# Performance work log

Hardware: AMD Instinct MI355X
Metric: run time of the kernel (lower is better)

Reference implementation:

```python
import jax, jax.numpy as jnp
import numpy as np

E = 256
H = 512
LN_EPS = 1e-5
NORM_EPS = 1e-12


def setup_inputs() -> dict:
    key = jax.random.key(0)
    ks = jax.random.split(key, 8)
    B, N, M = 8, 128, 128
    track_features = jax.random.normal(ks[0], (B, N, E), dtype=jnp.float32)
    det_features = jax.random.normal(ks[1], (B, M, E), dtype=jnp.float32)
    # MLP params (torch Linear default init style: uniform, but values irrelevant for correctness harness)
    lim1 = 1.0 / np.sqrt(3 * E)
    W1 = jax.random.uniform(ks[2], (3 * E, H), minval=-lim1, maxval=lim1, dtype=jnp.float32)
    b1 = jax.random.uniform(ks[3], (H,), minval=-lim1, maxval=lim1, dtype=jnp.float32)
    gamma = jnp.ones((H,), dtype=jnp.float32)
    beta = jnp.zeros((H,), dtype=jnp.float32)
    lim2 = 1.0 / np.sqrt(H)
    W2 = jax.random.uniform(ks[4], (H, 1), minval=-lim2, maxval=lim2, dtype=jnp.float32)
    b2 = jax.random.uniform(ks[5], (1,), minval=-lim2, maxval=lim2, dtype=jnp.float32)
    return {"track_features": track_features, "det_features": det_features,
            "W1": W1, "b1": b1, "gamma": gamma, "beta": beta, "W2": W2, "b2": b2}


def _l2_normalize(x):
    # F.normalize(x, dim=-1): x / max(||x||_2, eps)
    n = jnp.sqrt(jnp.sum(x * x, axis=-1, keepdims=True))
    return x / jnp.maximum(n, NORM_EPS)


def reference(track_features, det_features, W1, b1, gamma, beta, W2, b2):
    t = _l2_normalize(track_features)   # (B, N, E)
    d = _l2_normalize(det_features)     # (B, M, E)
    tb = t[:, :, None, :]               # (B, N, 1, E)
    db = d[:, None, :, :]               # (B, 1, M, E)
    B, N, _ = t.shape
    M = d.shape[1]
    diff = jnp.abs(tb - db)                                  # (B, N, M, E)
    pair = jnp.concatenate([jnp.broadcast_to(tb, (B, N, M, E)),
                            jnp.broadcast_to(db, (B, N, M, E)),
                            diff], axis=-1)                  # (B, N, M, 3E)
    h = jnp.einsum('bnme,eh->bnmh', pair, W1) + b1           # (B, N, M, H)
    mu = jnp.mean(h, axis=-1, keepdims=True)
    var = jnp.mean((h - mu) ** 2, axis=-1, keepdims=True)
    h = (h - mu) * jax.lax.rsqrt(var + LN_EPS) * gamma + beta
    h = h * jax.nn.sigmoid(h)                                # SiLU
    out = jnp.einsum('bnmh,ho->bnmo', h, W2)[..., 0] + b2[0]  # (B, N, M)
    return out
```

## Files before the change

### kernel.cpp

```cpp
#include <hip/hip_runtime.h>
#include <hip/hip_bf16.h>
#include <cstdint>

typedef __bf16 bf16x8 __attribute__((ext_vector_type(8)));
typedef __bf16 bf16x2 __attribute__((ext_vector_type(2)));
typedef float f32x4 __attribute__((ext_vector_type(4)));
typedef float f32x2 __attribute__((ext_vector_type(2)));

#define E_DIM 256
#define H_DIM 512

static __device__ __forceinline__ unsigned pkbf(float a, float b) {
    bf16x2 h;
    h[0] = (__bf16)a;
    h[1] = (__bf16)b;
    return __builtin_bit_cast(unsigned, h);
}

__global__ __launch_bounds__(512, 2)
void prep_kernel(const float* __restrict__ track, const float* __restrict__ det,
                 const float* __restrict__ W1, const float* __restrict__ b1,
                 float* __restrict__ P, float* __restrict__ Q,
                 __bf16* __restrict__ W1cc, float* __restrict__ sclT,
                 float* __restrict__ sclD, float* __restrict__ out) {
    __shared__ __align__(16) __bf16 Ash[16 * 256];
    int tid = threadIdx.x;
    int blk = blockIdx.x;

    if (blk >= 288) {
        int u = (blk - 288) * 512 + tid;
        float4 z = {0.f, 0.f, 0.f, 0.f};
#pragma unroll
        for (int i = 0; i < 4; ++i)
            ((float4*)out)[u + 8192 * i] = z;
        return;
    }
    if (blk >= 256) {
        int u = (blk - 256) * 512 + tid;
        int j = u & 3;
        int h = (u >> 2) & 511;
        int c = u >> 11;
        const float* src = W1 + (size_t)(512 + c * 32 + j * 8) * H_DIM + h;
        uint4 v;
        v.x = pkbf(src[0],                 src[(size_t)1 * H_DIM]);
        v.y = pkbf(src[(size_t)2 * H_DIM], src[(size_t)3 * H_DIM]);
        v.z = pkbf(src[(size_t)4 * H_DIM], src[(size_t)5 * H_DIM]);
        v.w = pkbf(src[(size_t)6 * H_DIM], src[(size_t)7 * H_DIM]);
        *(uint4*)(W1cc + ((size_t)(c * 512 + h) * 32 + j * 8)) = v;
        return;
    }

    int lane = tid & 63;
    int wave = tid >> 6;
    int lq   = lane >> 4;
    int lc   = lane & 15;
    int l5   = lane & 31;

    int mat  = blk >> 7;
    int rowg = (blk >> 1) & 63;
    int half = blk & 1;
    int r0   = rowg * 16;
    int h0   = half * 256;
    const float* src = mat ? det : track;

    {
        int row = wave * 2 + (lane >> 5);
        const float* gp = src + (size_t)(r0 + row) * E_DIM + l5 * 8;
        float4 x0 = *(const float4*)gp;
        float4 x1 = *(const float4*)(gp + 4);
        float ss = x0.x*x0.x + x0.y*x0.y + x0.z*x0.z + x0.w*x0.w
                 + x1.x*x1.x + x1.y*x1.y + x1.z*x1.z + x1.w*x1.w;
#pragma unroll
        for (int off = 16; off > 0; off >>= 1) ss += __shfl_xor(ss, off);
        float st = 1.0f / fmaxf(sqrtf(ss), 1e-12f);
        if (half == 0 && l5 == 0) (mat ? sclD : sclT)[r0 + row] = st;
        uint4 v;
        v.x = pkbf(x0.x * st, x0.y * st);
        v.y = pkbf(x0.z * st, x0.w * st);
        v.z = pkbf(x1.x * st, x1.y * st);
        v.w = pkbf(x1.z * st, x1.w * st);
        int cc = l5 >> 2, j = l5 & 3;
        *(uint4*)&Ash[(size_t)(cc * 64 + j * 16 + row) * 8] = v;
    }
    __syncthreads();

    int hB = h0 + wave * 32 + lc;
    const float* wb = W1 + (size_t)(mat * 256) * H_DIM + hB;
    float wf[2][8];
#pragma unroll
    for (int ht = 0; ht < 2; ++ht)
#pragma unroll
        for (int i = 0; i < 8; ++i)
            wf[ht][i] = wb[(size_t)(lq * 8 + i) * H_DIM + ht * 16];

    f32x4 acc[2];
    acc[0] = (f32x4){0.f, 0.f, 0.f, 0.f};
    acc[1] = (f32x4){0.f, 0.f, 0.f, 0.f};

#pragma unroll
    for (int c = 0; c < 8; ++c) {
        bf16x8 cw[2];
#pragma unroll
        for (int ht = 0; ht < 2; ++ht) {
            uint4 u;
            u.x = pkbf(wf[ht][0], wf[ht][1]);
            u.y = pkbf(wf[ht][2], wf[ht][3]);
            u.z = pkbf(wf[ht][4], wf[ht][5]);
            u.w = pkbf(wf[ht][6], wf[ht][7]);
            cw[ht] = __builtin_bit_cast(bf16x8, u);
        }
        if (c < 7) {
            const float* nb = wb + (size_t)((c + 1) * 32 + lq * 8) * H_DIM;
#pragma unroll
            for (int ht = 0; ht < 2; ++ht)
#pragma unroll
                for (int i = 0; i < 8; ++i)
                    wf[ht][i] = nb[(size_t)i * H_DIM + ht * 16];
        }
        bf16x8 af = *(const bf16x8*)&Ash[(size_t)(c * 64 + lane) * 8];
#pragma unroll
        for (int ht = 0; ht < 2; ++ht)
            acc[ht] = __builtin_amdgcn_mfma_f32_16x16x32_bf16(cw[ht], af, acc[ht], 0, 0, 0);
    }

    float* dst = mat ? Q : P;
#pragma unroll
    for (int ht = 0; ht < 2; ++ht) {
        int h = h0 + wave * 32 + ht * 16 + lq * 4;
        f32x4 o = acc[ht];
        if (!mat) o += *(const f32x4*)&b1[h];
        *(f32x4*)&dst[(size_t)(r0 + lc) * H_DIM + h] = o;
    }
}

__global__ __launch_bounds__(512, 4)
void main_kernel(const float* __restrict__ track, const float* __restrict__ det,
                 const __bf16* __restrict__ W1cc,
                 const float* __restrict__ P, const float* __restrict__ Q,
                 const float* __restrict__ sclT, const float* __restrict__ sclD,
                 const float* __restrict__ gamma, const float* __restrict__ beta,
                 const float* __restrict__ W2, const float* __restrict__ b2,
                 float* __restrict__ out) {
    __shared__ __align__(16) char SMEM[44032];
    __bf16* Ash  = (__bf16*)SMEM;
    float*  LNr1 = (float*)(SMEM + 32768);
    float*  LNr2 = (float*)(SMEM + 35072);
    float*  AS   = (float*)(SMEM + 37376);
    float*  BS   = (float*)(SMEM + 37632);
    float*  Gs   = (float*)(SMEM + 37888);
    float*  Bs   = (float*)(SMEM + 39936);
    float*  Ws   = (float*)(SMEM + 41984);

    int tid  = threadIdx.x;
    int lane = tid & 63;
    int wave = tid >> 6;
    int lq   = lane >> 4;
    int lc   = lane & 15;

    int i   = blockIdx.x;
    int xcd = i & 7;
    int t8  = (i >> 3) & 31;
    int b   = i >> 8;
    int n0  = ((xcd >> 1) * 4 + (t8 >> 3)) * 8;
    int m0  = ((xcd & 1) * 8 + (t8 & 7)) * 8;
    int gn  = b * 128 + n0;
    int gm  = b * 128 + m0;

    float b2v = b2[0];
    Gs[tid] = gamma[tid];
    Bs[tid] = beta[tid];
    Ws[tid] = W2[tid];

    const uint4* Wg = (const uint4*)W1cc;
    int hb = wave * 64 + lc;
    bf16x8 bwA[4], bwB[4];
#pragma unroll
    for (int ht = 0; ht < 4; ++ht)
        bwA[ht] = __builtin_bit_cast(bf16x8, Wg[(hb + ht * 16) * 4 + lq]);

    int k0 = wave * 32 + lq * 8;
    int ml = lane & 7;
    float sd = sclD[gm + ml];
    const float* dr = det + (size_t)(gm + ml) * E_DIM + k0;
    float4 d0 = *(const float4*)dr;
    float4 d1 = *(const float4*)(dr + 4);
#pragma unroll
    for (int r = 0; r < 4; ++r) {
        int nl = r * 2 + (lc >> 3);
        float st = sclT[gn + nl];
        const float* tr = track + (size_t)(gn + nl) * E_DIM + k0;
        float4 t0 = *(const float4*)tr;
        float4 t1 = *(const float4*)(tr + 4);
        uint4 v;
        v.x = pkbf(fabsf(t0.x * st - d0.x * sd), fabsf(t0.y * st - d0.y * sd));
        v.y = pkbf(fabsf(t0.z * st - d0.z * sd), fabsf(t0.w * st - d0.w * sd));
        v.z = pkbf(fabsf(t1.x * st - d1.x * sd), fabsf(t1.y * st - d1.y * sd));
        v.w = pkbf(fabsf(t1.z * st - d1.z * sd), fabsf(t1.w * st - d1.w * sd));
        *(uint4*)&Ash[(size_t)(r * 512 + wave * 64 + lane) * 8] = v;
    }

    const float* Pb = P + (size_t)gn * H_DIM;
    const float* Qb = Q + (size_t)gm * H_DIM;
    f32x4 acc[4][4];
    {
        f32x4 qv[4];
#pragma unroll
        for (int ht = 0; ht < 4; ++ht)
            qv[ht] = *(const f32x4*)&Qb[(size_t)ml * H_DIM + wave * 64 + ht * 16 + lq * 4];
#pragma unroll
        for (int pt = 0; pt < 4; ++pt) {
            int n = pt * 2 + (lc >> 3);
#pragma unroll
            for (int ht = 0; ht < 4; ++ht) {
                f32x4 pv = *(const f32x4*)&Pb[(size_t)n * H_DIM + wave * 64 + ht * 16 + lq * 4];
                acc[pt][ht] = pv + qv[ht];
            }
        }
    }
    __syncthreads();

#pragma unroll 2
    for (int c = 0; c < 8; ++c) {
        bf16x8* cur = (c & 1) ? bwB : bwA;
        bf16x8* nxt = (c & 1) ? bwA : bwB;
        int c1 = (c + 1) & 7;
#pragma unroll
        for (int ht = 0; ht < 4; ++ht)
            nxt[ht] = __builtin_bit_cast(bf16x8, Wg[c1 * 2048 + (hb + ht * 16) * 4 + lq]);
        __builtin_amdgcn_s_setprio(1);
#pragma unroll
        for (int pt = 0; pt < 4; ++pt) {
            bf16x8 af = *(const bf16x8*)&Ash[(size_t)((pt * 8 + c) * 64 + lane) * 8];
#pragma unroll
            for (int ht = 0; ht < 4; ++ht)
                acc[pt][ht] = __builtin_amdgcn_mfma_f32_16x16x32_bf16(cur[ht], af, acc[pt][ht], 0, 0, 0);
        }
        __builtin_amdgcn_s_setprio(0);
    }

#pragma unroll
    for (int pt = 0; pt < 4; ++pt) {
        f32x2 s1v = (f32x2){0.f, 0.f}, s2v = (f32x2){0.f, 0.f};
#pragma unroll
        for (int ht = 0; ht < 4; ++ht) {
#pragma unroll
            for (int hf = 0; hf < 2; ++hf) {
                f32x2 v = (f32x2){acc[pt][ht][hf * 2], acc[pt][ht][hf * 2 + 1]};
                s1v += v;
                s2v += v * v;
            }
        }
        float s1 = s1v[0] + s1v[1];
        float s2 = s2v[0] + s2v[1];
        s1 += __shfl_xor(s1, 16); s2 += __shfl_xor(s2, 16);
        s1 += __shfl_xor(s1, 32); s2 += __shfl_xor(s2, 32);
        if (lq == 0) {
            LNr1[(pt * 16 + lc) * 9 + wave] = s1;
            LNr2[(pt * 16 + lc) * 9 + wave] = s2;
        }
    }
    __syncthreads();
    {
        int p = tid >> 3, w = tid & 7;
        float s1 = LNr1[p * 9 + w];
        float s2 = LNr2[p * 9 + w];
        s1 += __shfl_xor(s1, 1); s2 += __shfl_xor(s2, 1);
        s1 += __shfl_xor(s1, 2); s2 += __shfl_xor(s2, 2);
        s1 += __shfl_xor(s1, 4); s2 += __shfl_xor(s2, 4);
        if (w == 0) {
            float mu  = s1 * (1.0f / 512.0f);
            float var = s2 * (1.0f / 512.0f) - mu * mu;
            float rs  = rsqrtf(var + 1e-5f);
            AS[p] = rs;
            BS[p] = -mu * rs;
        }
    }
    __syncthreads();

    float as[4], bs[4];
#pragma unroll
    for (int pt = 0; pt < 4; ++pt) { as[pt] = AS[pt * 16 + lc]; bs[pt] = BS[pt * 16 + lc]; }
    f32x2 cav[4];
#pragma unroll
    for (int pt = 0; pt < 4; ++pt) cav[pt] = (f32x2){0.f, 0.f};
#pragma unroll
    for (int ht = 0; ht < 4; ++ht) {
        int h = wave * 64 + ht * 16 + lq * 4;
        f32x4 g  = *(const f32x4*)&Gs[h];
        f32x4 bb = *(const f32x4*)&Bs[h];
        f32x4 w  = *(const f32x4*)&Ws[h];
#pragma unroll
        for (int pt = 0; pt < 4; ++pt) {
            f32x2 a2  = (f32x2){as[pt], as[pt]};
            f32x2 b2p = (f32x2){bs[pt], bs[pt]};
#pragma unroll
            for (int hf = 0; hf < 2; ++hf) {
                f32x2 v  = (f32x2){acc[pt][ht][hf * 2], acc[pt][ht][hf * 2 + 1]};
                f32x2 gg = (f32x2){g[hf * 2],  g[hf * 2 + 1]};
                f32x2 bv = (f32x2){bb[hf * 2], bb[hf * 2 + 1]};
                f32x2 wv = (f32x2){w[hf * 2],  w[hf * 2 + 1]};
                f32x2 x  = (v * a2 + b2p) * gg + bv;
                f32x2 xw = x * wv;
                f32x2 e, sg;
                e[0]  = __expf(-x[0]);
                e[1]  = __expf(-x[1]);
                sg[0] = __builtin_amdgcn_rcpf(1.0f + e[0]);
                sg[1] = __builtin_amdgcn_rcpf(1.0f + e[1]);
                cav[pt] += xw * sg;
            }
        }
    }
#pragma unroll
    for (int pt = 0; pt < 4; ++pt) {
        float cg = cav[pt][0] + cav[pt][1];
        cg += __shfl_xor(cg, 16);
        cg += __shfl_xor(cg, 32);
        if (lq == 0) {
            if (wave == 0) cg += b2v;
            int n = pt * 2 + (lc >> 3);
            int m = lc & 7;
            atomicAdd(&out[(size_t)(gn + n) * 128 + m0 + m], cg);
        }
    }
}

extern "C" void kernel_launch(void* const* d_in, const int* in_sizes, int n_in,
                              void* d_out, int out_size, void* d_ws, size_t ws_size,
                              hipStream_t stream) {
    const float* track = (const float*)d_in[0];
    const float* det   = (const float*)d_in[1];
    const float* W1    = (const float*)d_in[2];
    const float* b1    = (const float*)d_in[3];
    const float* gamma = (const float*)d_in[4];
    const float* beta  = (const float*)d_in[5];
    const float* W2    = (const float*)d_in[6];
    const float* b2    = (const float*)d_in[7];
    float* out = (float*)d_out;

    char* ws = (char*)d_ws;
    float*  Pp   = (float*)(ws);
    float*  Qp   = (float*)(ws + (2u << 20));
    __bf16* W1cc = (__bf16*)(ws + (4u << 20));
    float*  sclT = (float*)(ws + (4u << 20) + (256u << 10));
    float*  sclD = (float*)(ws + (4u << 20) + (264u << 10));

    prep_kernel<<<304, 512, 0, stream>>>(track, det, W1, b1, Pp, Qp, W1cc, sclT, sclD, out);
    main_kernel<<<2048, 512, 0, stream>>>(track, det, W1cc, Pp, Qp, sclT, sclD,
                                          gamma, beta, W2, b2, out);
}
```

Before: 142.9 us.

## Make main kernel persistent over four m-tiles with LDS-staged P/Q prefetch

Each block now processes four consecutive 8-column m-tiles instead of one, cutting the grid from 2048 to 512 blocks. The P rows and per-block constants are loaded once and reused across tiles. P and Q go into padded LDS through global_load_lds, and the next tile's Q is prefetched during the current tile's MFMA loop. LDS grows to about 77KB per block, which may lower occupancy, and 512 blocks give fewer waves to hide latency.

```diff
diff --git a/kernel.cpp b/kernel.cpp
--- a/kernel.cpp
+++ b/kernel.cpp
@@ -9,12 +9,19 @@
 
 #define E_DIM 256
 #define H_DIM 512
+#define PST 516
 
 static __device__ __forceinline__ unsigned pkbf(float a, float b) {
     bf16x2 h;
     h[0] = (__bf16)a;
     h[1] = (__bf16)b;
     return __builtin_bit_cast(unsigned, h);
+}
+
+static __device__ __forceinline__ void gl_lds16(const float* g, float* l) {
+    __builtin_amdgcn_global_load_lds(
+        (const __attribute__((address_space(1))) void*)g,
+        (__attribute__((address_space(3))) void*)l, 16, 0, 0);
 }
 
 __global__ __launch_bounds__(512, 2)
@@ -141,7 +148,7 @@
                  const float* __restrict__ gamma, const float* __restrict__ beta,
                  const float* __restrict__ W2, const float* __restrict__ b2,
                  float* __restrict__ out) {
-    __shared__ __align__(16) char SMEM[44032];
+    __shared__ __align__(16) char SMEM[77056];
     __bf16* Ash  = (__bf16*)SMEM;
     float*  LNr1 = (float*)(SMEM + 32768);
     float*  LNr2 = (float*)(SMEM + 35072);
@@ -150,27 +157,39 @@
     float*  Gs   = (float*)(SMEM + 37888);
     float*  Bs   = (float*)(SMEM + 39936);
     float*  Ws   = (float*)(SMEM + 41984);
+    float*  Psh  = (float*)(SMEM + 44032);
+    float*  Qsh  = (float*)(SMEM + 60544);
 
     int tid  = threadIdx.x;
     int lane = tid & 63;
     int wave = tid >> 6;
     int lq   = lane >> 4;
     int lc   = lane & 15;
-
-    int i   = blockIdx.x;
-    int xcd = i & 7;
-    int t8  = (i >> 3) & 31;
-    int b   = i >> 8;
-    int n0  = ((xcd >> 1) * 4 + (t8 >> 3)) * 8;
-    int m0  = ((xcd & 1) * 8 + (t8 & 7)) * 8;
-    int gn  = b * 128 + n0;
-    int gm  = b * 128 + m0;
+    int ml   = lane & 7;
+
+    int id  = blockIdx.x;
+    int xcd = id & 7;
+    int u   = id >> 3;
+    int b   = u >> 3;
+    int v   = u & 7;
+    int gn  = b * 128 + ((xcd >> 1) * 4 + (v >> 1)) * 8;
+    int mtb = (xcd & 1) * 8 + (v & 1) * 4;
 
     float b2v = b2[0];
     Gs[tid] = gamma[tid];
     Bs[tid] = beta[tid];
     Ws[tid] = W2[tid];
 
+    {
+        const float* gp = P + (size_t)(gn + wave) * H_DIM + lane * 4;
+        gl_lds16(gp,       Psh + wave * PST);
+        gl_lds16(gp + 256, Psh + wave * PST + 256);
+        int gm0 = b * 128 + mtb * 8;
+        const float* gq = Q + (size_t)(gm0 + wave) * H_DIM + lane * 4;
+        gl_lds16(gq,       Qsh + wave * PST);
+        gl_lds16(gq + 256, Qsh + wave * PST + 256);
+    }
+
     const uint4* Wg = (const uint4*)W1cc;
     int hb = wave * 64 + lc;
     bf16x8 bwA[4], bwB[4];
@@ -178,148 +197,167 @@
     for (int ht = 0; ht < 4; ++ht)
         bwA[ht] = __builtin_bit_cast(bf16x8, Wg[(hb + ht * 16) * 4 + lq]);
 
-    int k0 = wave * 32 + lq * 8;
-    int ml = lane & 7;
-    float sd = sclD[gm + ml];
-    const float* dr = det + (size_t)(gm + ml) * E_DIM + k0;
-    float4 d0 = *(const float4*)dr;
-    float4 d1 = *(const float4*)(dr + 4);
-#pragma unroll
-    for (int r = 0; r < 4; ++r) {
-        int nl = r * 2 + (lc >> 3);
-        float st = sclT[gn + nl];
-        const float* tr = track + (size_t)(gn + nl) * E_DIM + k0;
-        float4 t0 = *(const float4*)tr;
-        float4 t1 = *(const float4*)(tr + 4);
-        uint4 v;
-        v.x = pkbf(fabsf(t0.x * st - d0.x * sd), fabsf(t0.y * st - d0.y * sd));
-        v.y = pkbf(fabsf(t0.z * st - d0.z * sd), fabsf(t0.w * st - d0.w * sd));
-        v.z = pkbf(fabsf(t1.x * st - d1.x * sd), fabsf(t1.y * st - d1.y * sd));
-        v.w = pkbf(fabsf(t1.z * st - d1.z * sd), fabsf(t1.w * st - d1.w * sd));
-        *(uint4*)&Ash[(size_t)(r * 512 + wave * 64 + lane) * 8] = v;
-    }
-
-    const float* Pb = P + (size_t)gn * H_DIM;
-    const float* Qb = Q + (size_t)gm * H_DIM;
-    f32x4 acc[4][4];
-    {
-        f32x4 qv[4];
-#pragma unroll
-        for (int ht = 0; ht < 4; ++ht)
-            qv[ht] = *(const f32x4*)&Qb[(size_t)ml * H_DIM + wave * 64 + ht * 16 + lq * 4];
+    float stv[4];
+#pragma unroll
+    for (int r = 0; r < 4; ++r)
+        stv[r] = sclT[gn + r * 2 + (lc >> 3)];
+
+    asm volatile("s_waitcnt vmcnt(0)" ::: "memory");
+    __syncthreads();
+
+    for (int j = 0; j < 4; ++j) {
+        int gm = b * 128 + (mtb + j) * 8;
+
+        {
+            int k0 = wave * 32 + lq * 8;
+            float sd = sclD[gm + ml];
+            const float* dr = det + (size_t)(gm + ml) * E_DIM + k0;
+            float4 d0 = *(const float4*)dr;
+            float4 d1 = *(const float4*)(dr + 4);
+#pragma unroll
+            for (int r = 0; r < 4; ++r) {
+                int nl = r * 2 + (lc >> 3);
+                float st = stv[r];
+                const float* tr = track + (size_t)(gn + nl) * E_DIM + k0;
+                float4 t0 = *(const float4*)tr;
+                float4 t1 = *(const float4*)(tr + 4);
+                uint4 w;
+                w.x = pkbf(fabsf(t0.x * st - d0.x * sd), fabsf(t0.y * st - d0.y * sd));
+                w.y = pkbf(fabsf(t0.z * st - d0.z * sd), fabsf(t0.w * st - d0.w * sd));
+                w.z = pkbf(fabsf(t1.x * st - d1.x * sd), fabsf(t1.y * st - d1.y * sd));
+                w.w = pkbf(fabsf(t1.z * st - d1.z * sd), fabsf(t1.w * st - d1.w * sd));
+                *(uint4*)&Ash[(size_t)(r * 512 + wave * 64 + lane) * 8] = w;
+            }
+        }
+
+        f32x4 acc[4][4];
+        {
+            f32x4 qv[4];
+#pragma unroll
+            for (int ht = 0; ht < 4; ++ht)
+                qv[ht] = *(const f32x4*)&Qsh[ml * PST + wave * 64 + ht * 16 + lq * 4];
+#pragma unroll
+            for (int pt = 0; pt < 4; ++pt) {
+                int n = pt * 2 + (lc >> 3);
+#pragma unroll
+                for (int ht = 0; ht < 4; ++ht) {
+                    f32x4 pv = *(const f32x4*)&Psh[n * PST + wave * 64 + ht * 16 + lq * 4];
+                    acc[pt][ht] = pv + qv[ht];
+                }
+            }
+        }
+        __syncthreads();
+
+        if (j < 3) {
+            int gmn = b * 128 + (mtb + j + 1) * 8;
+            const float* gq = Q + (size_t)(gmn + wave) * H_DIM + lane * 4;
+            gl_lds16(gq,       Qsh + wave * PST);
+            gl_lds16(gq + 256, Qsh + wave * PST + 256);
+        }
+
+#pragma unroll 2
+        for (int c = 0; c < 8; ++c) {
+            bf16x8* cur = (c & 1) ? bwB : bwA;
+            bf16x8* nxt = (c & 1) ? bwA : bwB;
+            int c1 = (c + 1) & 7;
+#pragma unroll
+            for (int ht = 0; ht < 4; ++ht)
+                nxt[ht] = __builtin_bit_cast(bf16x8, Wg[c1 * 2048 + (hb + ht * 16) * 4 + lq]);
+            __builtin_amdgcn_s_setprio(1);
+#pragma unroll
+            for (int pt = 0; pt < 4; ++pt) {
+                bf16x8 af = *(const bf16x8*)&Ash[(size_t)((pt * 8 + c) * 64 + lane) * 8];
+#pragma unroll
+                for (int ht = 0; ht < 4; ++ht)
+                    acc[pt][ht] = __builtin_amdgcn_mfma_f32_16x16x32_bf16(cur[ht], af, acc[pt][ht], 0, 0, 0);
+            }
+            __builtin_amdgcn_s_setprio(0);
+        }
+
 #pragma unroll
         for (int pt = 0; pt < 4; ++pt) {
-            int n = pt * 2 + (lc >> 3);
+            f32x2 s1v = (f32x2){0.f, 0.f}, s2v = (f32x2){0.f, 0.f};
 #pragma unroll
             for (int ht = 0; ht < 4; ++ht) {
-                f32x4 pv = *(const f32x4*)&Pb[(size_t)n * H_DIM + wave * 64 + ht * 16 + lq * 4];
-                acc[pt][ht] = pv + qv[ht];
-            }
-        }
-    }
-    __syncthreads();
-
-#pragma unroll 2
-    for (int c = 0; c < 8; ++c) {
-        bf16x8* cur = (c & 1) ? bwB : bwA;
-        bf16x8* nxt = (c & 1) ? bwA : bwB;
-        int c1 = (c + 1) & 7;
-#pragma unroll
-        for (int ht = 0; ht < 4; ++ht)
-            nxt[ht] = __builtin_bit_cast(bf16x8, Wg[c1 * 2048 + (hb + ht * 16) * 4 + lq]);
-        __builtin_amdgcn_s_setprio(1);
+#pragma unroll
+                for (int hf = 0; hf < 2; ++hf) {
+                    f32x2 vv = (f32x2){acc[pt][ht][hf * 2], acc[pt][ht][hf * 2 + 1]};
+                    s1v += vv;
+                    s2v += vv * vv;
+                }
+            }
+            float s1 = s1v[0] + s1v[1];
+            float s2 = s2v[0] + s2v[1];
+            s1 += __shfl_xor(s1, 16); s2 += __shfl_xor(s2, 16);
+            s1 += __shfl_xor(s1, 32); s2 += __shfl_xor(s2, 32);
+            if (lq == 0) {
+                LNr1[(pt * 16 + lc) * 9 + wave] = s1;
+                LNr2[(pt * 16 + lc) * 9 + wave] = s2;
+            }
+        }
+        __syncthreads();
+        {
+            int p = tid >> 3, w = tid & 7;
+            float s1 = LNr1[p * 9 + w];
+            float s2 = LNr2[p * 9 + w];
+            s1 += __shfl_xor(s1, 1); s2 += __shfl_xor(s2, 1);
+            s1 += __shfl_xor(s1, 2); s2 += __shfl_xor(s2, 2);
+            s1 += __shfl_xor(s1, 4); s2 += __shfl_xor(s2, 4);
+            if (w == 0) {
+                float mu  = s1 * (1.0f / 512.0f);
+                float var = s2 * (1.0f / 512.0f) - mu * mu;
+                float rs  = rsqrtf(var + 1e-5f);
+                AS[p] = rs;
+                BS[p] = -mu * rs;
+            }
+        }
+        asm volatile("s_waitcnt vmcnt(0)" ::: "memory");
+        __syncthreads();
+
+        float as[4], bs[4];
+#pragma unroll
+        for (int pt = 0; pt < 4; ++pt) { as[pt] = AS[pt * 16 + lc]; bs[pt] = BS[pt * 16 + lc]; }
+        f32x2 cav[4];
+#pragma unroll
+        for (int pt = 0; pt < 4; ++pt) cav[pt] = (f32x2){0.f, 0.f};
+#pragma unroll
+        for (int ht = 0; ht < 4; ++ht) {
+            int h = wave * 64 + ht * 16 + lq * 4;
+            f32x4 g  = *(const f32x4*)&Gs[h];
+            f32x4 bb = *(const f32x4*)&Bs[h];
+            f32x4 w  = *(const f32x4*)&Ws[h];
+#pragma unroll
+            for (int pt = 0; pt < 4; ++pt) {
+                f32x2 a2  = (f32x2){as[pt], as[pt]};
+                f32x2 b2p = (f32x2){bs[pt], bs[pt]};
+#pragma unroll
+                for (int hf = 0; hf < 2; ++hf) {
+                    f32x2 vv = (f32x2){acc[pt][ht][hf * 2], acc[pt][ht][hf * 2 + 1]};
+                    f32x2 gg = (f32x2){g[hf * 2],  g[hf * 2 + 1]};
+                    f32x2 bv = (f32x2){bb[hf * 2], bb[hf * 2 + 1]};
+                    f32x2 wv = (f32x2){w[hf * 2],  w[hf * 2 + 1]};
+                    f32x2 x  = (vv * a2 + b2p) * gg + bv;
+                    f32x2 xw = x * wv;
+                    f32x2 e, sg;
+                    e[0]  = __expf(-x[0]);
+                    e[1]  = __expf(-x[1]);
+                    sg[0] = __builtin_amdgcn_rcpf(1.0f + e[0]);
+                    sg[1] = __builtin_amdgcn_rcpf(1.0f + e[1]);
+                    cav[pt] += xw * sg;
+                }
+            }
+        }
 #pragma unroll
         for (int pt = 0; pt < 4; ++pt) {
-            bf16x8 af = *(const bf16x8*)&Ash[(size_t)((pt * 8 + c) * 64 + lane) * 8];
-#pragma unroll
-            for (int ht = 0; ht < 4; ++ht)
-                acc[pt][ht] = __builtin_amdgcn_mfma_f32_16x16x32_bf16(cur[ht], af, acc[pt][ht], 0, 0, 0);
-        }
-        __builtin_amdgcn_s_setprio(0);
-    }
-
-#pragma unroll
-    for (int pt = 0; pt < 4; ++pt) {
-        f32x2 s1v = (f32x2){0.f, 0.f}, s2v = (f32x2){0.f, 0.f};
-#pragma unroll
-        for (int ht = 0; ht < 4; ++ht) {
-#pragma unroll
-            for (int hf = 0; hf < 2; ++hf) {
-                f32x2 v = (f32x2){acc[pt][ht][hf * 2], acc[pt][ht][hf * 2 + 1]};
-                s1v += v;
-                s2v += v * v;
-            }
-        }
-        float s1 = s1v[0] + s1v[1];
-        float s2 = s2v[0] + s2v[1];
-        s1 += __shfl_xor(s1, 16); s2 += __shfl_xor(s2, 16);
-        s1 += __shfl_xor(s1, 32); s2 += __shfl_xor(s2, 32);
-        if (lq == 0) {
-            LNr1[(pt * 16 + lc) * 9 + wave] = s1;
-            LNr2[(pt * 16 + lc) * 9 + wave] = s2;
-        }
-    }
-    __syncthreads();
-    {
-        int p = tid >> 3, w = tid & 7;
-        float s1 = LNr1[p * 9 + w];
-        float s2 = LNr2[p * 9 + w];
-        s1 += __shfl_xor(s1, 1); s2 += __shfl_xor(s2, 1);
-        s1 += __shfl_xor(s1, 2); s2 += __shfl_xor(s2, 2);
-        s1 += __shfl_xor(s1, 4); s2 += __shfl_xor(s2, 4);
-        if (w == 0) {
-            float mu  = s1 * (1.0f / 512.0f);
-            float var = s2 * (1.0f / 512.0f) - mu * mu;
-            float rs  = rsqrtf(var + 1e-5f);
-            AS[p] = rs;
-            BS[p] = -mu * rs;
-        }
-    }
-    __syncthreads();
-
-    float as[4], bs[4];
-#pragma unroll
-    for (int pt = 0; pt < 4; ++pt) { as[pt] = AS[pt * 16 + lc]; bs[pt] = BS[pt * 16 + lc]; }
-    f32x2 cav[4];
-#pragma unroll
-    for (int pt = 0; pt < 4; ++pt) cav[pt] = (f32x2){0.f, 0.f};
-#pragma unroll
-    for (int ht = 0; ht < 4; ++ht) {
-        int h = wave * 64 + ht * 16 + lq * 4;
-        f32x4 g  = *(const f32x4*)&Gs[h];
-        f32x4 bb = *(const f32x4*)&Bs[h];
-        f32x4 w  = *(const f32x4*)&Ws[h];
-#pragma unroll
-        for (int pt = 0; pt < 4; ++pt) {
-            f32x2 a2  = (f32x2){as[pt], as[pt]};
-            f32x2 b2p = (f32x2){bs[pt], bs[pt]};
-#pragma unroll
-            for (int hf = 0; hf < 2; ++hf) {
-                f32x2 v  = (f32x2){acc[pt][ht][hf * 2], acc[pt][ht][hf * 2 + 1]};
-                f32x2 gg = (f32x2){g[hf * 2],  g[hf * 2 + 1]};
-                f32x2 bv = (f32x2){bb[hf * 2], bb[hf * 2 + 1]};
-                f32x2 wv = (f32x2){w[hf * 2],  w[hf * 2 + 1]};
-                f32x2 x  = (v * a2 + b2p) * gg + bv;
-                f32x2 xw = x * wv;
-                f32x2 e, sg;
-                e[0]  = __expf(-x[0]);
-                e[1]  = __expf(-x[1]);
-                sg[0] = __builtin_amdgcn_rcpf(1.0f + e[0]);
-                sg[1] = __builtin_amdgcn_rcpf(1.0f + e[1]);
-                cav[pt] += xw * sg;
-            }
-        }
-    }
-#pragma unroll
-    for (int pt = 0; pt < 4; ++pt) {
-        float cg = cav[pt][0] + cav[pt][1];
-        cg += __shfl_xor(cg, 16);
-        cg += __shfl_xor(cg, 32);
-        if (lq == 0) {
-            if (wave == 0) cg += b2v;
-            int n = pt * 2 + (lc >> 3);
-            int m = lc & 7;
-            atomicAdd(&out[(size_t)(gn + n) * 128 + m0 + m], cg);
+            float cg = cav[pt][0] + cav[pt][1];
+            cg += __shfl_xor(cg, 16);
+            cg += __shfl_xor(cg, 32);
+            if (lq == 0) {
+                if (wave == 0) cg += b2v;
+                int n = pt * 2 + (lc >> 3);
+                int m = lc & 7;
+                atomicAdd(&out[(size_t)(gn + n) * 128 + (mtb + j) * 8 + m], cg);
+            }
         }
     }
 }
@@ -345,6 +383,6 @@
     float*  sclD = (float*)(ws + (4u << 20) + (264u << 10));
 
     prep_kernel<<<304, 512, 0, stream>>>(track, det, W1, b1, Pp, Qp, W1cc, sclT, sclD, out);
-    main_kernel<<<2048, 512, 0, stream>>>(track, det, W1cc, Pp, Qp, sclT, sclD,
-                                          gamma, beta, W2, b2, out);
-}
+    main_kernel<<<512, 512, 0, stream>>>(track, det, W1cc, Pp, Qp, sclT, sclD,
+                                         gamma, beta, W2, b2, out);
+}
```

New measurement: 180.0 us. 25.9% more time.

## Split prep kernel across 512 blocks and fold W1 convert and zeroing in

Applied to the files above, without the earlier changes.

The prep kernel now launches 512 blocks, each computing a quarter of the hidden dimension (128 columns) instead of half, so every wave does one MFMA tile instead of two. The separate blocks that converted the diff-part of W1 to bf16 and zeroed the output are removed, and that work is spread across the first 96 threads of every block. This aims to fill more CUs in the short prep phase and drop the imbalanced tail blocks. The cost is that each row block's normalization is now recomputed four times instead of twice.

```diff
diff --git a/kernel.cpp b/kernel.cpp
--- a/kernel.cpp
+++ b/kernel.cpp
@@ -24,44 +24,37 @@
                  __bf16* __restrict__ W1cc, float* __restrict__ sclT,
                  float* __restrict__ sclD, float* __restrict__ out) {
     __shared__ __align__(16) __bf16 Ash[16 * 256];
-    int tid = threadIdx.x;
-    int blk = blockIdx.x;
-
-    if (blk >= 288) {
-        int u = (blk - 288) * 512 + tid;
-        float4 z = {0.f, 0.f, 0.f, 0.f};
-#pragma unroll
-        for (int i = 0; i < 4; ++i)
-            ((float4*)out)[u + 8192 * i] = z;
-        return;
-    }
-    if (blk >= 256) {
-        int u = (blk - 256) * 512 + tid;
-        int j = u & 3;
-        int h = (u >> 2) & 511;
-        int c = u >> 11;
-        const float* src = W1 + (size_t)(512 + c * 32 + j * 8) * H_DIM + h;
-        uint4 v;
-        v.x = pkbf(src[0],                 src[(size_t)1 * H_DIM]);
-        v.y = pkbf(src[(size_t)2 * H_DIM], src[(size_t)3 * H_DIM]);
-        v.z = pkbf(src[(size_t)4 * H_DIM], src[(size_t)5 * H_DIM]);
-        v.w = pkbf(src[(size_t)6 * H_DIM], src[(size_t)7 * H_DIM]);
-        *(uint4*)(W1cc + ((size_t)(c * 512 + h) * 32 + j * 8)) = v;
-        return;
-    }
-
+    int tid  = threadIdx.x;
+    int blk  = blockIdx.x;
     int lane = tid & 63;
     int wave = tid >> 6;
     int lq   = lane >> 4;
     int lc   = lane & 15;
     int l5   = lane & 31;
 
-    int mat  = blk >> 7;
-    int rowg = (blk >> 1) & 63;
-    int half = blk & 1;
+    int mat  = blk >> 8;
+    int rowg = (blk >> 2) & 63;
+    int hq   = blk & 3;
     int r0   = rowg * 16;
-    int h0   = half * 256;
+    int h0   = hq * 128;
     const float* src = mat ? det : track;
+
+    if (tid < 32) {
+        int u = blk * 32 + tid;
+        int j = u & 3;
+        int h = (u >> 2) & 511;
+        int c = u >> 11;
+        const float* s = W1 + (size_t)(512 + c * 32 + j * 8) * H_DIM + h;
+        uint4 v;
+        v.x = pkbf(s[0],                 s[(size_t)1 * H_DIM]);
+        v.y = pkbf(s[(size_t)2 * H_DIM], s[(size_t)3 * H_DIM]);
+        v.z = pkbf(s[(size_t)4 * H_DIM], s[(size_t)5 * H_DIM]);
+        v.w = pkbf(s[(size_t)6 * H_DIM], s[(size_t)7 * H_DIM]);
+        *(uint4*)(W1cc + ((size_t)(c * 512 + h) * 32 + j * 8)) = v;
+    } else if (tid < 96) {
+        float4 z = {0.f, 0.f, 0.f, 0.f};
+        ((float4*)out)[blk * 64 + (tid - 32)] = z;
+    }
 
     {
         int row = wave * 2 + (lane >> 5);
@@ -73,7 +66,7 @@
 #pragma unroll
         for (int off = 16; off > 0; off >>= 1) ss += __shfl_xor(ss, off);
         float st = 1.0f / fmaxf(sqrtf(ss), 1e-12f);
-        if (half == 0 && l5 == 0) (mat ? sclD : sclT)[r0 + row] = st;
+        if (hq == 0 && l5 == 0) (mat ? sclD : sclT)[r0 + row] = st;
         uint4 v;
         v.x = pkbf(x0.x * st, x0.y * st);
         v.y = pkbf(x0.z * st, x0.w * st);
@@ -84,53 +77,38 @@
     }
     __syncthreads();
 
-    int hB = h0 + wave * 32 + lc;
+    int hB = h0 + wave * 16 + lc;
     const float* wb = W1 + (size_t)(mat * 256) * H_DIM + hB;
-    float wf[2][8];
-#pragma unroll
-    for (int ht = 0; ht < 2; ++ht)
-#pragma unroll
-        for (int i = 0; i < 8; ++i)
-            wf[ht][i] = wb[(size_t)(lq * 8 + i) * H_DIM + ht * 16];
-
-    f32x4 acc[2];
-    acc[0] = (f32x4){0.f, 0.f, 0.f, 0.f};
-    acc[1] = (f32x4){0.f, 0.f, 0.f, 0.f};
+    float wf[8];
+#pragma unroll
+    for (int i = 0; i < 8; ++i)
+        wf[i] = wb[(size_t)(lq * 8 + i) * H_DIM];
+
+    f32x4 acc = (f32x4){0.f, 0.f, 0.f, 0.f};
 
 #pragma unroll
     for (int c = 0; c < 8; ++c) {
-        bf16x8 cw[2];
-#pragma unroll
-        for (int ht = 0; ht < 2; ++ht) {
-            uint4 u;
-            u.x = pkbf(wf[ht][0], wf[ht][1]);
-            u.y = pkbf(wf[ht][2], wf[ht][3]);
-            u.z = pkbf(wf[ht][4], wf[ht][5]);
-            u.w = pkbf(wf[ht][6], wf[ht][7]);
-            cw[ht] = __builtin_bit_cast(bf16x8, u);
-        }
+        uint4 u;
+        u.x = pkbf(wf[0], wf[1]);
+        u.y = pkbf(wf[2], wf[3]);
+        u.z = pkbf(wf[4], wf[5]);
+        u.w = pkbf(wf[6], wf[7]);
+        bf16x8 cw = __builtin_bit_cast(bf16x8, u);
         if (c < 7) {
             const float* nb = wb + (size_t)((c + 1) * 32 + lq * 8) * H_DIM;
 #pragma unroll
-            for (int ht = 0; ht < 2; ++ht)
-#pragma unroll
-                for (int i = 0; i < 8; ++i)
-                    wf[ht][i] = nb[(size_t)i * H_DIM + ht * 16];
+            for (int i = 0; i < 8; ++i)
+                wf[i] = nb[(size_t)i * H_DIM];
         }
         bf16x8 af = *(const bf16x8*)&Ash[(size_t)(c * 64 + lane) * 8];
-#pragma unroll
-        for (int ht = 0; ht < 2; ++ht)
-            acc[ht] = __builtin_amdgcn_mfma_f32_16x16x32_bf16(cw[ht], af, acc[ht], 0, 0, 0);
+        acc = __builtin_amdgcn_mfma_f32_16x16x32_bf16(cw, af, acc, 0, 0, 0);
     }
 
     float* dst = mat ? Q : P;
-#pragma unroll
-    for (int ht = 0; ht < 2; ++ht) {
-        int h = h0 + wave * 32 + ht * 16 + lq * 4;
-        f32x4 o = acc[ht];
-        if (!mat) o += *(const f32x4*)&b1[h];
-        *(f32x4*)&dst[(size_t)(r0 + lc) * H_DIM + h] = o;
-    }
+    int h = h0 + wave * 16 + lq * 4;
+    f32x4 o = acc;
+    if (!mat) o += *(const f32x4*)&b1[h];
+    *(f32x4*)&dst[(size_t)(r0 + lc) * H_DIM + h] = o;
 }
 
 __global__ __launch_bounds__(512, 4)
@@ -344,7 +322,7 @@
     float*  sclT = (float*)(ws + (4u << 20) + (256u << 10));
     float*  sclD = (float*)(ws + (4u << 20) + (264u << 10));
 
-    prep_kernel<<<304, 512, 0, stream>>>(track, det, W1, b1, Pp, Qp, W1cc, sclT, sclD, out);
+    prep_kernel<<<512, 512, 0, stream>>>(track, det, W1, b1, Pp, Qp, W1cc, sclT, sclD, out);
     main_kernel<<<2048, 512, 0, stream>>>(track, det, W1cc, Pp, Qp, sclT, sclD,
                                           gamma, beta, W2, b2, out);
 }
```

After: 142.2 us (median of 2 runs). No clear change (-0.5%).
